# Kernel optimization log

Measured on AMD Instinct MI355X. Metric: run time of the kernel, lower is better.

The kernel has to match this reference:

```python
import jax, jax.numpy as jnp
import numpy as np

H = 8   # num_heads
K = 2   # num_timescales (hard-coded in module)


def _apply_rope(x, cos, sin):
    # x: [B,T,H,D]; cos/sin: [1,T,1,D/2]; interleaved even/odd pairs
    xp = x.reshape(*x.shape[:-1], -1, 2)
    xr, xi = xp[..., 0], xp[..., 1]
    rr = xr * cos - xi * sin
    ri = xr * sin + xi * cos
    return jnp.stack([rr, ri], axis=-1).reshape(x.shape)


def setup_inputs() -> dict:
    key = jax.random.key(0)
    ks = jax.random.split(key, 11)
    B, T, C = 4, 2048, 1024
    HK = H * K
    s = 0.02  # xavier-ish scale
    return {
        'x': jax.random.normal(ks[0], (B, T, C), jnp.float32),
        'mask': jnp.ones((B, T), jnp.int32),
        'Wq': jax.random.normal(ks[1], (C, C), jnp.float32) * s,
        'Wk': jax.random.normal(ks[2], (C, C), jnp.float32) * s,
        'Wv': jax.random.normal(ks[3], (C, C), jnp.float32) * s,
        'Wb': jax.random.normal(ks[4], (C, HK), jnp.float32) * s,
        'bb': jax.random.normal(ks[5], (HK,), jnp.float32) * 0.5 + 2.0,
        'Wm': jax.random.normal(ks[6], (C, HK), jnp.float32) * s,
        'bm': jax.random.normal(ks[7], (HK,), jnp.float32) * 0.1,
        'Wo': jax.random.normal(ks[8], (C, C), jnp.float32) * s,
        'bo': jnp.zeros((C,), jnp.float32),
    }


def reference(x, mask, Wq, Wk, Wv, Wb, bb, Wm, bm, Wo, bo):
    B, T, C = x.shape
    D = C // H
    q = (x @ Wq).reshape(B, T, H, D)
    k = (x @ Wk).reshape(B, T, H, D)
    v = (x @ Wv).reshape(B, T, H, D)

    # RoPE cache
    inv_freq = 1.0 / (10000.0 ** (jnp.arange(0, D, 2, dtype=jnp.float32) / D))
    freqs = jnp.arange(T, dtype=jnp.float32)[:, None] * inv_freq[None, :]  # [T,D/2]
    cos = jnp.cos(freqs)[None, :, None, :].astype(x.dtype)
    sin = jnp.sin(freqs)[None, :, None, :].astype(x.dtype)
    q = _apply_rope(q, cos, sin)
    k = _apply_rope(k, cos, sin)

    beta = jax.nn.sigmoid((x @ Wb + bb).reshape(B, T, H, K))  # [B,T,H,K]
    mix = jax.nn.softmax((x @ Wm + bm).reshape(B, T, H, K), axis=-1)

    def step(S, ins):
        # S: [B,H,K,D,D]
        q_t, k_t, v_t, b_t, m_t, mk = ins  # [B,H,D],[B,H,D],[B,H,D],[B,H,K],[B,H,K],[B]
        outer = jnp.einsum('bhd,bhe->bhde', k_t, v_t)          # [B,H,D,D]
        S_new = b_t[..., None, None] * S + outer[:, :, None]   # [B,H,K,D,D]
        S = jnp.where(mk[:, None, None, None, None] > 0, S_new, S)
        y_k = jnp.einsum('bhd,bhkde->bhke', q_t, S)            # [B,H,K,D]
        y_t = jnp.sum(y_k * m_t[..., None], axis=2)            # [B,H,D]
        y_t = jnp.where(mk[:, None, None] > 0, y_t, jnp.zeros_like(y_t))
        return S, y_t

    S0 = jnp.zeros((B, H, K, D, D), x.dtype)
    xs = (jnp.swapaxes(q, 0, 1), jnp.swapaxes(k, 0, 1), jnp.swapaxes(v, 0, 1),
          jnp.swapaxes(beta, 0, 1), jnp.swapaxes(mix, 0, 1), mask.T)
    _, ys = jax.lax.scan(step, S0, xs)           # ys: [T,B,H,D]
    y = jnp.swapaxes(ys, 0, 1).reshape(B, T, C)
    return y @ Wo + bo
```

## Files before the change

### kernel.cpp

```cpp
#include <hip/hip_runtime.h>

typedef __attribute__((ext_vector_type(4))) float f32x4;
typedef __attribute__((ext_vector_type(8))) __bf16 bf16x8;

#define T_DIM 2048
#define B_DIM 4
#define C_DIM 1024
#define H_N 8
#define D_H 128
#define M_ROWS 8192
#define MC ((size_t)M_ROWS * C_DIM)
#define LCH 64
#define NCH (T_DIM / LCH)
#define CHSZ (128 * 128)
#define SWE(r) ((((r) ^ ((r) >> 3)) & 7) << 3)

#define GLDS16(g, l) __builtin_amdgcn_global_load_lds( \
    (const __attribute__((address_space(1))) void*)(g), \
    (__attribute__((address_space(3))) void*)(l), 16, 0, 0)

__global__ __launch_bounds__(256) void prep_all_k(
    const float* __restrict__ x, __bf16* __restrict__ xb,
    const float* __restrict__ W0, const float* __restrict__ W1,
    const float* __restrict__ W2, const float* __restrict__ W3,
    __bf16* __restrict__ WT,
    float2* __restrict__ tab,
    const float* __restrict__ Wb, const float* __restrict__ Wm,
    __bf16* __restrict__ WbmT) {
    __shared__ float t[64][65];
    int bid = blockIdx.x;
    int tid = threadIdx.x;
    if (bid < 4096) {
        int i = bid * 256 + tid;
        f32x4 a = ((const f32x4*)x)[i * 2];
        f32x4 b = ((const f32x4*)x)[i * 2 + 1];
        bf16x8 o;
        o[0] = (__bf16)a.x; o[1] = (__bf16)a.y; o[2] = (__bf16)a.z; o[3] = (__bf16)a.w;
        o[4] = (__bf16)b.x; o[5] = (__bf16)b.y; o[6] = (__bf16)b.z; o[7] = (__bf16)b.w;
        ((bf16x8*)xb)[i] = o;
    } else if (bid < 5120) {
        int tt = bid - 4096;
        int wz = tt >> 8, rem = tt & 255;
        int r0 = (rem >> 4) * 64, c0 = (rem & 15) * 64;
        const float* W = wz == 0 ? W0 : wz == 1 ? W1 : wz == 2 ? W2 : W3;
        __bf16* o = WT + (size_t)wz * C_DIM * C_DIM;
        #pragma unroll
        for (int it = 0; it < 4; ++it) {
            int idx = it * 256 + tid;
            int r = idx >> 4, c4 = (idx & 15) * 4;
            f32x4 v = *(const f32x4*)(W + (size_t)(r0 + r) * C_DIM + c0 + c4);
            t[r][c4] = v.x; t[r][c4 + 1] = v.y; t[r][c4 + 2] = v.z; t[r][c4 + 3] = v.w;
        }
        __syncthreads();
        #pragma unroll
        for (int it = 0; it < 2; ++it) {
            int idx = it * 256 + tid;
            int n = idx >> 3, k8 = (idx & 7) * 8;
            bf16x8 ov;
            #pragma unroll
            for (int j = 0; j < 8; ++j) ov[j] = (__bf16)t[k8 + j][n];
            *(bf16x8*)(o + (size_t)(c0 + n) * C_DIM + r0 + k8) = ov;
        }
    } else {
        int sp = bid - 5120;
        if (sp < 512) {
            int idx = sp * 256 + tid;
            int tq = idx >> 6, i = idx & 63;
            float freq = expf(-(2.0f * (float)i / 128.0f) * 9.210340371976184f);
            float a = (float)tq * freq;
            tab[idx] = make_float2(cosf(a), sinf(a));
        } else {
            int n = sp - 512;
            int col = n & 15;
            const float* W = (n < 16) ? Wb : Wm;
            for (int k = tid; k < C_DIM; k += 256)
                WbmT[(size_t)n * C_DIM + k] = (__bf16)W[(size_t)k * 16 + col];
        }
    }
}

__global__ __launch_bounds__(256) void betamix_mfma(
    const __bf16* __restrict__ xb, const __bf16* __restrict__ WbmT,
    const float* __restrict__ bb, const float* __restrict__ bm,
    float* __restrict__ beta, float* __restrict__ mix) {
    __shared__ __bf16 As[2][32 * 64];

    int tid = threadIdx.x;
    int w = tid >> 6, lane = tid & 63;
    int lr = lane & 15, lg = lane >> 4;
    int ifr = w >> 1, j = w & 1;
    int rows0 = blockIdx.x * 32;

    int srow = tid >> 3;
    int sg = (tid & 7) ^ (srow & 7);
    size_t aoff = (size_t)(rows0 + srow) * C_DIM + sg * 8;
    int ldso = w * 64 * 16;

    f32x4 acc = {};
    const __bf16* Wrow = WbmT + (size_t)(j * 16 + lr) * C_DIM;

    GLDS16(xb + aoff, (char*)As[0] + ldso);
    asm volatile("s_waitcnt vmcnt(0)" ::: "memory");
    __syncthreads();

    for (int t = 0; t < 16; ++t) {
        int cur = t & 1;
        if (t < 15) GLDS16(xb + aoff + (t + 1) * 64, (char*)As[cur ^ 1] + ldso);
        #pragma unroll
        for (int ss = 0; ss < 2; ++ss) {
            int ar = ifr * 16 + lr;
            bf16x8 af = *(const bf16x8*)((char*)As[cur] + ar * 128 + (((ss * 4 + lg) ^ (ar & 7)) << 4));
            bf16x8 bf = *(const bf16x8*)(Wrow + t * 64 + ss * 32 + lg * 8);
            acc = __builtin_amdgcn_mfma_f32_16x16x32_bf16(af, bf, acc, 0, 0, 0);
        }
        asm volatile("s_waitcnt vmcnt(0)" ::: "memory");
        __syncthreads();
    }

    float bias = (j ? bm : bb)[lr];
    #pragma unroll
    for (int r = 0; r < 4; ++r) {
        int row = rows0 + ifr * 16 + lg * 4 + r;
        float v = acc[r] + bias;
        if (j == 0) {
            beta[(size_t)row * 16 + lr] = 1.f / (1.f + expf(-v));
        } else {
            float other = __shfl_xor(v, 1);
            float mx = fmaxf(v, other);
            float e = expf(v - mx), eo = expf(other - mx);
            mix[(size_t)row * 16 + lr] = e / (e + eo);
        }
    }
}

__global__ __launch_bounds__(256) void decay_k(
    const float* __restrict__ beta, const float* __restrict__ mixp,
    const int* __restrict__ mask,
    float* __restrict__ wvm, float* __restrict__ rcm,
    float* __restrict__ qsc, float* __restrict__ cumLg) {
    int gw = blockIdx.x * 4 + (threadIdx.x >> 6);
    int s = threadIdx.x & 63;
    int scan = gw >> 5, c = gw & 31;
    int b = scan >> 4, hh = scan & 15;
    size_t row = (size_t)b * T_DIM + c * LCH + s;
    int mk = mask[row];
    float mf = mk ? 1.f : 0.f;
    float bt = mk ? beta[row * 16 + hh] : 1.f;
    float mx = mk ? mixp[row * 16 + hh] : 0.f;
    float cum = bt;
    #pragma unroll
    for (int off = 1; off < 64; off <<= 1) {
        float p = __shfl(cum, (s >= off) ? s - off : 0);
        if (s >= off) cum *= p;
    }
    float cl = __shfl(cum, 63);
    size_t o = (size_t)scan * T_DIM + c * LCH + s;
    wvm[o] = mf * cl / cum;
    rcm[o] = mf / cum;
    qsc[o] = mf * mx * cum;
    if (s == 63) cumLg[scan * NCH + c] = cl;
}

__global__ __launch_bounds__(256) void gemm_qkv(
    const __bf16* __restrict__ A, const __bf16* __restrict__ BT,
    __bf16* __restrict__ outq, const float2* __restrict__ rope_tab) {
    __shared__ __bf16 As[128 * 64];
    __shared__ __bf16 Bs[128 * 64];
    const int K = C_DIM;

    int tid = threadIdx.x;
    int xcd = blockIdx.x & 7, lid = blockIdx.x >> 3;
    int g = lid >> 6, u = lid & 63;
    int bm = xcd * 8 + (u >> 3), bn = g * 8 + (u & 7);
    int m_base = bm << 7, n_base = bn << 7;
    int w = tid >> 6, lane = tid & 63;
    int lr = lane & 15, lg = lane >> 4;
    int wm = (w >> 1) * 64, wn = (w & 1) * 64;

    size_t aoff[4], boff[4];
    int ldso[4];
    #pragma unroll
    for (int it = 0; it < 4; ++it) {
        int gi = it * 256 + tid;
        int row = gi >> 3;
        int gr = (gi & 7) ^ (row & 7);
        aoff[it] = (size_t)(m_base + row) * K + gr * 8;
        boff[it] = (size_t)(n_base + row) * K + gr * 8;
        ldso[it] = (it * 256 + w * 64) * 16;
    }

    f32x4 acc[4][4] = {};

    for (int k0 = 0; k0 < K; k0 += 64) {
        __syncthreads();
        #pragma unroll
        for (int it = 0; it < 4; ++it) {
            GLDS16(A + aoff[it] + k0, (char*)As + ldso[it]);
            GLDS16(BT + boff[it] + k0, (char*)Bs + ldso[it]);
        }
        __syncthreads();
        #pragma unroll
        for (int ss = 0; ss < 2; ++ss) {
            bf16x8 af[4], bfr[4];
            #pragma unroll
            for (int i = 0; i < 4; ++i) {
                int ar = wm + i * 16 + lr;
                af[i] = *(const bf16x8*)((char*)As + ar * 128 + (((ss * 4 + lg) ^ (ar & 7)) << 4));
                int br = wn + i * 16 + lr;
                bfr[i] = *(const bf16x8*)((char*)Bs + br * 128 + (((ss * 4 + lg) ^ (br & 7)) << 4));
            }
            #pragma unroll
            for (int i = 0; i < 4; ++i)
                #pragma unroll
                for (int j = 0; j < 4; ++j)
                    acc[i][j] = __builtin_amdgcn_mfma_f32_16x16x32_bf16(af[i], bfr[j], acc[i][j], 0, 0, 0);
        }
    }

    #pragma unroll
    for (int i = 0; i < 4; ++i) {
        #pragma unroll
        for (int j = 0; j < 4; ++j) {
            #pragma unroll
            for (int r = 0; r < 4; ++r) {
                int grow = m_base + wm + i * 16 + (lg << 2) + r;
                int gcol = n_base + wn + j * 16 + lr;
                float val = acc[i][j][r];
                int buf = gcol >> 10;
                int col = gcol & 1023;
                if (buf < 2) {
                    float partner = __shfl_xor(val, 1);
                    int t = grow & (T_DIM - 1);
                    int ii = (col & 127) >> 1;
                    float2 cs = rope_tab[t * 64 + ii];
                    val = (col & 1) ? (partner * cs.y + val * cs.x)
                                    : (val * cs.x - partner * cs.y);
                }
                outq[(size_t)buf * MC + (size_t)grow * C_DIM + col] = (__bf16)val;
            }
        }
    }
}

__global__ __launch_bounds__(256) void gemm_out64(
    const __bf16* __restrict__ A, const __bf16* __restrict__ BT,
    float* __restrict__ Cp, const float* __restrict__ bias) {
    __shared__ __bf16 As[64 * 64];
    __shared__ __bf16 Bs[128 * 64];
    const int K = C_DIM, N = C_DIM;

    int tid = threadIdx.x;
    int bid = ((int)blockIdx.x & 7) * 128 + ((int)blockIdx.x >> 3);
    int bm = bid >> 3, bn = bid & 7;
    int m_base = bm << 6, n_base = bn << 7;
    int w = tid >> 6, lane = tid & 63;
    int lr = lane & 15, lg = lane >> 4;
    int wm = (w >> 1) * 32, wn = (w & 1) * 64;

    size_t aoff[2], boff[4];
    int ldsoA[2], ldsoB[4];
    #pragma unroll
    for (int it = 0; it < 2; ++it) {
        int gi = it * 256 + tid;
        int row = gi >> 3;
        int g = (gi & 7) ^ (row & 7);
        aoff[it] = (size_t)(m_base + row) * K + g * 8;
        ldsoA[it] = (it * 256 + w * 64) * 16;
    }
    #pragma unroll
    for (int it = 0; it < 4; ++it) {
        int gi = it * 256 + tid;
        int row = gi >> 3;
        int g = (gi & 7) ^ (row & 7);
        boff[it] = (size_t)(n_base + row) * K + g * 8;
        ldsoB[it] = (it * 256 + w * 64) * 16;
    }

    f32x4 acc[2][4] = {};

    for (int k0 = 0; k0 < K; k0 += 64) {
        __syncthreads();
        #pragma unroll
        for (int it = 0; it < 2; ++it)
            GLDS16(A + aoff[it] + k0, (char*)As + ldsoA[it]);
        #pragma unroll
        for (int it = 0; it < 4; ++it)
            GLDS16(BT + boff[it] + k0, (char*)Bs + ldsoB[it]);
        __syncthreads();
        #pragma unroll
        for (int ss = 0; ss < 2; ++ss) {
            bf16x8 af[2], bfr[4];
            #pragma unroll
            for (int i = 0; i < 2; ++i) {
                int ar = wm + i * 16 + lr;
                af[i] = *(const bf16x8*)((char*)As + ar * 128 + (((ss * 4 + lg) ^ (ar & 7)) << 4));
            }
            #pragma unroll
            for (int j = 0; j < 4; ++j) {
                int br = wn + j * 16 + lr;
                bfr[j] = *(const bf16x8*)((char*)Bs + br * 128 + (((ss * 4 + lg) ^ (br & 7)) << 4));
            }
            #pragma unroll
            for (int i = 0; i < 2; ++i)
                #pragma unroll
                for (int j = 0; j < 4; ++j)
                    acc[i][j] = __builtin_amdgcn_mfma_f32_16x16x32_bf16(af[i], bfr[j], acc[i][j], 0, 0, 0);
        }
    }

    #pragma unroll
    for (int i = 0; i < 2; ++i) {
        #pragma unroll
        for (int j = 0; j < 4; ++j) {
            #pragma unroll
            for (int r = 0; r < 4; ++r) {
                int grow = m_base + wm + i * 16 + (lg << 2) + r;
                int gcol = n_base + wn + j * 16 + lr;
                Cp[(size_t)grow * N + gcol] = acc[i][j][r] + bias[gcol];
            }
        }
    }
}

__global__ __launch_bounds__(256) void chunk_sum_k(
    const __bf16* __restrict__ kg, const __bf16* __restrict__ vg,
    const float* __restrict__ wvm, __bf16* __restrict__ BT) {
    __shared__ __bf16 KT[128 * 64];
    __shared__ __bf16 VT[128 * 64];

    int tid = threadIdx.x;
    int c = blockIdx.x, kk = blockIdx.y, bh = blockIdx.z;
    int b = bh >> 3, h = bh & 7;
    int scan = bh * 2 + kk;
    size_t rowb = (size_t)b * T_DIM + c * LCH;
    size_t wb = (size_t)scan * T_DIM + c * LCH;

    #pragma unroll
    for (int it = 0; it < 4; ++it) {
        int f = tid + it * 256;
        int s = f >> 4, c8 = (f & 15) * 8;
        size_t g = (rowb + s) * C_DIM + h * D_H + c8;
        bf16x8 kv = *(const bf16x8*)(kg + g);
        bf16x8 vv = *(const bf16x8*)(vg + g);
        float ws_ = wvm[wb + s];
        #pragma unroll
        for (int j = 0; j < 8; ++j) {
            int d = c8 + j;
            KT[d * 64 + (s ^ SWE(d))] = (__bf16)(ws_ * (float)kv[j]);
            VT[d * 64 + (s ^ SWE(d))] = vv[j];
        }
    }
    __syncthreads();

    int w = tid >> 6, l = tid & 63;
    int lr = l & 15, lg = l >> 4;
    f32x4 acc[2][8] = {};
    #pragma unroll
    for (int kt = 0; kt < 2; ++kt) {
        int col = kt * 32 + lg * 8;
        bf16x8 aV[2], bK[8];
        #pragma unroll
        for (int et = 0; et < 2; ++et) {
            int e = w * 32 + et * 16 + lr;
            aV[et] = *(const bf16x8*)&VT[e * 64 + (col ^ SWE(e))];
        }
        #pragma unroll
        for (int dt = 0; dt < 8; ++dt) {
            int d = dt * 16 + lr;
            bK[dt] = *(const bf16x8*)&KT[d * 64 + (col ^ SWE(d))];
        }
        #pragma unroll
        for (int et = 0; et < 2; ++et)
            #pragma unroll
            for (int dt = 0; dt < 8; ++dt)
                acc[et][dt] = __builtin_amdgcn_mfma_f32_16x16x32_bf16(aV[et], bK[dt], acc[et][dt], 0, 0, 0);
    }

    __bf16* bout = BT + ((size_t)scan * NCH + c) * CHSZ;
    #pragma unroll
    for (int et = 0; et < 2; ++et)
        #pragma unroll
        for (int dt = 0; dt < 8; ++dt)
            #pragma unroll
            for (int r = 0; r < 4; ++r) {
                int e = w * 32 + et * 16 + lg * 4 + r;
                bout[e * 128 + dt * 16 + lr] = (__bf16)acc[et][dt][r];
            }
}

__global__ __launch_bounds__(256) void chunk_scan_k(
    __bf16* __restrict__ BT, const float* __restrict__ cumLg) {
    int bid = blockIdx.x;
    int scan = bid >> 3, part = bid & 7;
    int tid = threadIdx.x;
    int e = part * 16 + (tid >> 4);
    int d0 = (tid & 15) * 8;
    __bf16* base = BT + (size_t)scan * NCH * CHSZ + e * 128 + d0;
    const float* cl = cumLg + scan * NCH;
    float acc[8] = {};
    for (int c = 0; c < NCH; ++c) {
        bf16x8 bv = *(const bf16x8*)(base + (size_t)c * CHSZ);
        float g = cl[c];
        bf16x8 so;
        #pragma unroll
        for (int j = 0; j < 8; ++j) so[j] = (__bf16)acc[j];
        *(bf16x8*)(base + (size_t)c * CHSZ) = so;
        #pragma unroll
        for (int j = 0; j < 8; ++j) acc[j] = g * acc[j] + (float)bv[j];
    }
}

__global__ __launch_bounds__(256, 3) void chunk_out_k(
    const __bf16* __restrict__ qg, const __bf16* __restrict__ kg,
    const __bf16* __restrict__ vg, const __bf16* __restrict__ ST,
    const float* __restrict__ rcm, const float* __restrict__ qscg,
    __bf16* __restrict__ yg) {
    __shared__ __bf16 STs[2][64 * 128];
    __shared__ __bf16 VT[64 * 64];
    __shared__ __bf16 Ps[64 * 72];
    __shared__ float rcumf[2][64], qscf[2][64];

    int tid = threadIdx.x;
    int c = blockIdx.x, eh = blockIdx.y, bh = blockIdx.z;
    int b = bh >> 3, h = bh & 7;
    int e0 = eh * 64;
    size_t rowb = (size_t)b * T_DIM + c * LCH;
    int w = tid >> 6, l = tid & 63;
    int lr = l & 15, lg = l >> 4;

    {
        const __bf16* stb = ST + ((size_t)(bh * 2) * NCH + c) * CHSZ + (size_t)e0 * 128;
        int r = tid >> 4, gran = tid & 15;
        size_t goff = (size_t)r * 128 + ((gran ^ (r & 7)) * 8);
        #pragma unroll
        for (int kk = 0; kk < 2; ++kk) {
            const __bf16* sp = stb + (size_t)kk * NCH * CHSZ;
            #pragma unroll
            for (int it = 0; it < 4; ++it) {
                GLDS16(sp + goff + (size_t)it * 16 * 128,
                       (char*)STs[kk] + (it * 256 + w * 64) * 16);
            }
        }
    }

    if (tid < 128) {
        int s = tid & 63, kk = tid >> 6;
        size_t o = (size_t)(bh * 2 + kk) * T_DIM + c * LCH + s;
        rcumf[kk][s] = rcm[o];
        qscf[kk][s] = qscg[o];
    }

    bf16x8 vreg[2];
    #pragma unroll
    for (int it = 0; it < 2; ++it) {
        int f = tid + it * 256;
        int s = f >> 3, c8 = (f & 7) * 8;
        vreg[it] = *(const bf16x8*)(vg + (rowb + s) * C_DIM + h * D_H + e0 + c8);
    }

    const __bf16* qrow = qg + (rowb + w * 16 + lr) * C_DIM + h * D_H;
    bf16x8 aQ[4];
    #pragma unroll
    for (int kt = 0; kt < 4; ++kt)
        aQ[kt] = *(const bf16x8*)(qrow + kt * 32 + lg * 8);

    const __bf16* kbase = kg + rowb * C_DIM + h * D_H;
    bf16x8 bkreg[16];
    #pragma unroll
    for (int st = 0; st < 4; ++st)
        #pragma unroll
        for (int kt = 0; kt < 4; ++kt)
            bkreg[st * 4 + kt] = *(const bf16x8*)(kbase + (size_t)(st * 16 + lr) * C_DIM + kt * 32 + lg * 8);

    #pragma unroll
    for (int it = 0; it < 2; ++it) {
        int f = tid + it * 256;
        int s = f >> 3, c8 = (f & 7) * 8;
        #pragma unroll
        for (int j = 0; j < 8; ++j) {
            int el = c8 + j;
            VT[el * 64 + (s ^ SWE(el))] = vreg[it][j];
        }
    }

    f32x4 Praw[4];
    #pragma unroll
    for (int st = 0; st < 4; ++st) {
        f32x4 p = {};
        #pragma unroll
        for (int kt = 0; kt < 4; ++kt)
            p = __builtin_amdgcn_mfma_f32_16x16x32_bf16(aQ[kt], bkreg[st * 4 + kt], p, 0, 0, 0);
        Praw[st] = p;
    }

    asm volatile("s_waitcnt vmcnt(0)" ::: "memory");
    __syncthreads();

    f32x4 yA[4] = {};
    #pragma unroll
    for (int kk = 0; kk < 2; ++kk) {
        #pragma unroll
        for (int st = 0; st < 4; ++st) {
            #pragma unroll
            for (int r = 0; r < 4; ++r) {
                int tl = w * 16 + lg * 4 + r;
                int sc = st * 16 + lr;
                float pv = (sc <= tl) ? Praw[st][r] * rcumf[kk][sc] * qscf[kk][tl] : 0.f;
                Ps[tl * 72 + sc] = (__bf16)pv;
            }
        }
        bf16x8 aP[2];
        #pragma unroll
        for (int k2 = 0; k2 < 2; ++k2)
            aP[k2] = *(const bf16x8*)&Ps[(w * 16 + lr) * 72 + k2 * 32 + lg * 8];

        __builtin_amdgcn_s_setprio(1);
        #pragma unroll
        for (int et = 0; et < 4; ++et) {
            int el = et * 16 + lr;
            f32x4 ys = {};
            #pragma unroll
            for (int kt = 0; kt < 4; ++kt) {
                bf16x8 bs = *(const bf16x8*)((char*)STs[kk] + el * 256 + (((kt * 4 + lg) ^ (el & 7)) << 4));
                ys = __builtin_amdgcn_mfma_f32_16x16x32_bf16(aQ[kt], bs, ys, 0, 0, 0);
            }
            f32x4 yp = {};
            #pragma unroll
            for (int k2 = 0; k2 < 2; ++k2) {
                bf16x8 bv = *(const bf16x8*)&VT[el * 64 + ((k2 * 32 + lg * 8) ^ SWE(el))];
                yp = __builtin_amdgcn_mfma_f32_16x16x32_bf16(aP[k2], bv, yp, 0, 0, 0);
            }
            #pragma unroll
            for (int r = 0; r < 4; ++r)
                yA[et][r] += ys[r] * qscf[kk][w * 16 + lg * 4 + r] + yp[r];
        }
        __builtin_amdgcn_s_setprio(0);
    }
    #pragma unroll
    for (int et = 0; et < 4; ++et)
        #pragma unroll
        for (int r = 0; r < 4; ++r) {
            size_t row = rowb + w * 16 + lg * 4 + r;
            yg[row * C_DIM + h * D_H + e0 + et * 16 + lr] = (__bf16)yA[et][r];
        }
}

extern "C" void kernel_launch(void* const* d_in, const int* in_sizes, int n_in,
                              void* d_out, int out_size, void* d_ws, size_t ws_size,
                              hipStream_t stream) {
    const float* x    = (const float*)d_in[0];
    const int*   mask = (const int*)d_in[1];
    const float* Wq   = (const float*)d_in[2];
    const float* Wk   = (const float*)d_in[3];
    const float* Wv   = (const float*)d_in[4];
    const float* Wb   = (const float*)d_in[5];
    const float* bb   = (const float*)d_in[6];
    const float* Wm   = (const float*)d_in[7];
    const float* bm   = (const float*)d_in[8];
    const float* Wo   = (const float*)d_in[9];
    const float* bo   = (const float*)d_in[10];
    float* out = (float*)d_out;

    __bf16* q    = (__bf16*)d_ws;
    __bf16* k    = q + MC;
    __bf16* v    = k + MC;
    __bf16* xb   = v + MC;
    __bf16* WT   = xb + MC;
    __bf16* BT   = WT + (size_t)4 * C_DIM * C_DIM;
    float* beta  = (float*)(BT + (size_t)64 * NCH * CHSZ);
    float* mixb  = beta + M_ROWS * 16;
    float* cumL  = mixb + M_ROWS * 16;
    float* wvm   = cumL + 64 * NCH;
    float* rcm   = wvm + (size_t)64 * T_DIM;
    float* qscg  = rcm + (size_t)64 * T_DIM;
    float2* rope = (float2*)(qscg + (size_t)64 * T_DIM);
    __bf16* WbmT = (__bf16*)(rope + T_DIM * 64);
    __bf16* ysum = xb;

    prep_all_k<<<dim3(5664), dim3(256), 0, stream>>>(
        x, xb, Wq, Wk, Wv, Wo, WT, rope, Wb, Wm, WbmT);
    betamix_mfma<<<dim3(M_ROWS / 32), dim3(256), 0, stream>>>(xb, WbmT, bb, bm, beta, mixb);
    decay_k<<<dim3(512), dim3(256), 0, stream>>>(beta, mixb, mask, wvm, rcm, qscg, cumL);

    const size_t CC = (size_t)C_DIM * C_DIM;
    gemm_qkv<<<dim3(1536), dim3(256), 0, stream>>>(xb, WT, q, rope);

    chunk_sum_k<<<dim3(NCH, 2, 32), dim3(256), 0, stream>>>(k, v, wvm, BT);
    chunk_scan_k<<<dim3(512), dim3(256), 0, stream>>>(BT, cumL);
    chunk_out_k<<<dim3(NCH, 2, 32), dim3(256), 0, stream>>>(q, k, v, BT, rcm, qscg, ysum);

    gemm_out64<<<dim3(1024), dim3(256), 0, stream>>>(ysum, WT + 3 * CC, out, bo);
}
```

Baseline: 222.7 us.

## Enlarge QKV GEMM tiles to 256x256 with double-buffered LDS staging

The QKV projection GEMM moves from 128x128 tiles with 256 threads to 256x256 tiles with 512 threads, and each wave now owns a 128x64 sub-tile. LDS is double-buffered so the global-to-LDS load of the next K slice overlaps the MFMA work on the current one, and the MFMA section is wrapped in s_setprio. The larger tiles raise operand reuse and remove one barrier per K step. The cost is that only 384 blocks are launched, about 1.5 waves on the CUs, so the tail may sit partly idle. The 128KB LDS footprint also limits each CU to one block.

```diff
diff --git a/kernel.cpp b/kernel.cpp
--- a/kernel.cpp
+++ b/kernel.cpp
@@ -161,64 +161,77 @@
     if (s == 63) cumLg[scan * NCH + c] = cl;
 }
 
-__global__ __launch_bounds__(256) void gemm_qkv(
+__global__ __launch_bounds__(512, 2) void gemm_qkv256(
     const __bf16* __restrict__ A, const __bf16* __restrict__ BT,
     __bf16* __restrict__ outq, const float2* __restrict__ rope_tab) {
-    __shared__ __bf16 As[128 * 64];
-    __shared__ __bf16 Bs[128 * 64];
+    __shared__ __bf16 As[2][256 * 64];
+    __shared__ __bf16 Bs[2][256 * 64];
     const int K = C_DIM;
 
     int tid = threadIdx.x;
-    int xcd = blockIdx.x & 7, lid = blockIdx.x >> 3;
-    int g = lid >> 6, u = lid & 63;
-    int bm = xcd * 8 + (u >> 3), bn = g * 8 + (u & 7);
-    int m_base = bm << 7, n_base = bn << 7;
+    int bid = ((int)blockIdx.x & 7) * 48 + ((int)blockIdx.x >> 3);
+    int bm = bid / 12, bn = bid % 12;
+    int m_base = bm << 8, n_base = bn << 8;
     int w = tid >> 6, lane = tid & 63;
     int lr = lane & 15, lg = lane >> 4;
-    int wm = (w >> 1) * 64, wn = (w & 1) * 64;
+    int wr = w >> 2, wc = w & 3;
+    int wm = wr * 128, wn = wc * 64;
 
     size_t aoff[4], boff[4];
     int ldso[4];
     #pragma unroll
     for (int it = 0; it < 4; ++it) {
-        int gi = it * 256 + tid;
+        int gi = it * 512 + tid;
         int row = gi >> 3;
         int gr = (gi & 7) ^ (row & 7);
         aoff[it] = (size_t)(m_base + row) * K + gr * 8;
         boff[it] = (size_t)(n_base + row) * K + gr * 8;
-        ldso[it] = (it * 256 + w * 64) * 16;
-    }
-
-    f32x4 acc[4][4] = {};
-
-    for (int k0 = 0; k0 < K; k0 += 64) {
-        __syncthreads();
-        #pragma unroll
-        for (int it = 0; it < 4; ++it) {
-            GLDS16(A + aoff[it] + k0, (char*)As + ldso[it]);
-            GLDS16(BT + boff[it] + k0, (char*)Bs + ldso[it]);
-        }
-        __syncthreads();
-        #pragma unroll
-        for (int ss = 0; ss < 2; ++ss) {
-            bf16x8 af[4], bfr[4];
-            #pragma unroll
-            for (int i = 0; i < 4; ++i) {
+        ldso[it] = (it * 512 + w * 64) * 16;
+    }
+
+#define STAGE_Q(bufi, k0)                                                   \
+    _Pragma("unroll")                                                       \
+    for (int it = 0; it < 4; ++it) {                                        \
+        GLDS16(A + aoff[it] + (k0), (char*)As[bufi] + ldso[it]);            \
+        GLDS16(BT + boff[it] + (k0), (char*)Bs[bufi] + ldso[it]);           \
+    }
+
+    f32x4 acc[8][4] = {};
+
+    STAGE_Q(0, 0);
+    __syncthreads();
+
+    const int nt = K >> 6;
+    for (int t = 0; t < nt; ++t) {
+        int cur = t & 1;
+        if (t + 1 < nt) STAGE_Q(cur ^ 1, (t + 1) * 64);
+        #pragma unroll
+        for (int s = 0; s < 2; ++s) {
+            bf16x8 bfr[4], af[8];
+            #pragma unroll
+            for (int j = 0; j < 4; ++j) {
+                int br = wn + j * 16 + lr;
+                bfr[j] = *(const bf16x8*)((char*)Bs[cur] + br * 128 + (((s * 4 + lg) ^ (br & 7)) << 4));
+            }
+            #pragma unroll
+            for (int i = 0; i < 8; ++i) {
                 int ar = wm + i * 16 + lr;
-                af[i] = *(const bf16x8*)((char*)As + ar * 128 + (((ss * 4 + lg) ^ (ar & 7)) << 4));
-                int br = wn + i * 16 + lr;
-                bfr[i] = *(const bf16x8*)((char*)Bs + br * 128 + (((ss * 4 + lg) ^ (br & 7)) << 4));
-            }
-            #pragma unroll
-            for (int i = 0; i < 4; ++i)
+                af[i] = *(const bf16x8*)((char*)As[cur] + ar * 128 + (((s * 4 + lg) ^ (ar & 7)) << 4));
+            }
+            __builtin_amdgcn_s_setprio(1);
+            #pragma unroll
+            for (int i = 0; i < 8; ++i)
                 #pragma unroll
                 for (int j = 0; j < 4; ++j)
                     acc[i][j] = __builtin_amdgcn_mfma_f32_16x16x32_bf16(af[i], bfr[j], acc[i][j], 0, 0, 0);
-        }
-    }
-
-    #pragma unroll
-    for (int i = 0; i < 4; ++i) {
+            __builtin_amdgcn_s_setprio(0);
+        }
+        __syncthreads();
+    }
+#undef STAGE_Q
+
+    #pragma unroll
+    for (int i = 0; i < 8; ++i) {
         #pragma unroll
         for (int j = 0; j < 4; ++j) {
             #pragma unroll
@@ -583,7 +596,7 @@
     decay_k<<<dim3(512), dim3(256), 0, stream>>>(beta, mixb, mask, wvm, rcm, qscg, cumL);
 
     const size_t CC = (size_t)C_DIM * C_DIM;
-    gemm_qkv<<<dim3(1536), dim3(256), 0, stream>>>(xb, WT, q, rope);
+    gemm_qkv256<<<dim3(384), dim3(512), 0, stream>>>(xb, WT, q, rope);
 
     chunk_sum_k<<<dim3(NCH, 2, 32), dim3(256), 0, stream>>>(k, v, wvm, BT);
     chunk_scan_k<<<dim3(512), dim3(256), 0, stream>>>(BT, cumL);
```

After: 240.1 us. +7.8%, slower.
